# Kernel tuning notes

Hardware: AMD Instinct MI355X
Metric: run time of the kernel (lower is better)

## Reference

```python
import jax, jax.numpy as jnp
import numpy as np

B, OUT, IN = 1024, 512, 1024

def setup_inputs() -> dict:
    key = jax.random.key(0)
    k1, k2, k3, k4 = jax.random.split(key, 4)
    x = jax.random.uniform(k1, (B, IN), dtype=jnp.float32)            # inputs in [0,1]
    w = jax.random.uniform(k2, (OUT, IN), dtype=jnp.float32)          # centers in [min_input, max_input]=[0,1]
    u = jax.random.uniform(k3, (OUT, IN), dtype=jnp.float32, minval=0.2, maxval=0.7)  # slopes per init
    andor01 = jax.random.randint(k4, (1, OUT), 0, 2).astype(jnp.float32)  # frozen 0/1 mix ('*' mode)
    return {"x": x, "w": w, "u": u, "andor01": andor01}

def reference(x, w, u, andor01):
    # xuw = u * (x[b,None,i] - w[o,i]) ; z[b,o] = sum_i xuw^2 ; y = exp(-z)
    diff = u[None, :, :] * (x[:, None, :] - w[None, :, :])   # [B, OUT, IN]
    z = jnp.sum(diff * diff, axis=-1)                        # [B, OUT]
    y = jnp.exp(-z)                                          # forward of LargeAttractorExp
    # andor == '*': y + andor01 * (1 - 2y)
    return y + andor01 * (1.0 - 2.0 * y)
```

## Files before the change

kernel.cpp:

```cpp
#include <hip/hip_runtime.h>

#define B_SZ   1024
#define OUT_SZ 512
#define IN_SZ  1024
#define K2     2048
#define NKSTEP 65
#define MT     64
#define NT     32

typedef __bf16 bf16x8 __attribute__((ext_vector_type(8)));
typedef float  f32x4  __attribute__((ext_vector_type(4)));

#define A_ELEMS ((size_t)MT * NKSTEP * 64 * 8)
#define B_ELEMS ((size_t)NT * NKSTEP * 64 * 8)
#define OFF_B   (A_ELEMS * 2)
#define OFF_P   (A_ELEMS * 2 + B_ELEMS * 2)

__global__ __launch_bounds__(256) void rbf_prep_a(
    const float* __restrict__ x, __bf16* __restrict__ Ash)
{
    int t = blockIdx.x * 256 + threadIdx.x;
    int lane  = t & 63;
    int tmp   = t >> 6;
    int kStep = tmp % NKSTEP;
    int mTile = tmp / NKSTEP;
    int b     = mTile * 16 + (lane & 15);
    int quad  = lane >> 4;

    bf16x8 v;
    if (kStep < 64) {
        int kk = kStep * 32 + quad * 8;
        if (kk < IN_SZ) {
            const float4 f0 = *(const float4*)&x[(size_t)b * IN_SZ + kk];
            const float4 f1 = *(const float4*)&x[(size_t)b * IN_SZ + kk + 4];
            float f[8] = {f0.x, f0.y, f0.z, f0.w, f1.x, f1.y, f1.z, f1.w};
            #pragma unroll
            for (int j = 0; j < 8; ++j) v[j] = (__bf16)(f[j] * f[j]);
        } else {
            int i0 = kk - IN_SZ;
            const float4 f0 = *(const float4*)&x[(size_t)b * IN_SZ + i0];
            const float4 f1 = *(const float4*)&x[(size_t)b * IN_SZ + i0 + 4];
            float f[8] = {f0.x, f0.y, f0.z, f0.w, f1.x, f1.y, f1.z, f1.w};
            #pragma unroll
            for (int j = 0; j < 8; ++j) v[j] = (__bf16)f[j];
        }
    } else {
        #pragma unroll
        for (int j = 0; j < 8; ++j) v[j] = (__bf16)0.f;
        if (quad == 0) v[0] = (__bf16)1.f;
    }
    *(bf16x8*)&Ash[(size_t)t * 8] = v;
}

__global__ __launch_bounds__(256) void rbf_prep_b(
    const float* __restrict__ w, const float* __restrict__ u,
    __bf16* __restrict__ Bsh)
{
    int t = blockIdx.x * 256 + threadIdx.x;
    int lane  = t & 63;
    int tmp   = t >> 6;
    int kStep = tmp % NKSTEP;
    int nTile = tmp / NKSTEP;
    int o     = nTile * 16 + (lane & 15);
    int quad  = lane >> 4;

    bf16x8 v;
    if (kStep < 64) {
        int kk = kStep * 32 + quad * 8;
        if (kk < IN_SZ) {
            const float4 u0 = *(const float4*)&u[(size_t)o * IN_SZ + kk];
            const float4 u1 = *(const float4*)&u[(size_t)o * IN_SZ + kk + 4];
            float uf[8] = {u0.x, u0.y, u0.z, u0.w, u1.x, u1.y, u1.z, u1.w};
            #pragma unroll
            for (int j = 0; j < 8; ++j) v[j] = (__bf16)(uf[j] * uf[j]);
        } else {
            int i0 = kk - IN_SZ;
            const float4 u0 = *(const float4*)&u[(size_t)o * IN_SZ + i0];
            const float4 u1 = *(const float4*)&u[(size_t)o * IN_SZ + i0 + 4];
            const float4 w0 = *(const float4*)&w[(size_t)o * IN_SZ + i0];
            const float4 w1 = *(const float4*)&w[(size_t)o * IN_SZ + i0 + 4];
            float uf[8] = {u0.x, u0.y, u0.z, u0.w, u1.x, u1.y, u1.z, u1.w};
            float wf[8] = {w0.x, w0.y, w0.z, w0.w, w1.x, w1.y, w1.z, w1.w};
            #pragma unroll
            for (int j = 0; j < 8; ++j) v[j] = (__bf16)(-2.f * uf[j] * uf[j] * wf[j]);
        }
    } else {
        #pragma unroll
        for (int j = 0; j < 8; ++j) v[j] = (__bf16)0.f;
    }
    *(bf16x8*)&Bsh[(size_t)t * 8] = v;
}

__global__ __launch_bounds__(256) void rbf_prep_r(
    const float* __restrict__ w, const float* __restrict__ u,
    __bf16* __restrict__ Bsh)
{
    int wave = threadIdx.x >> 6;
    int lane = threadIdx.x & 63;
    int o    = blockIdx.x * 4 + wave;

    float s = 0.f;
    #pragma unroll
    for (int c = 0; c < 4; ++c) {
        int i = lane * 16 + c * 4;
        const float4 uv = *(const float4*)&u[(size_t)o * IN_SZ + i];
        const float4 wv = *(const float4*)&w[(size_t)o * IN_SZ + i];
        float t0 = uv.x * wv.x, t1 = uv.y * wv.y, t2 = uv.z * wv.z, t3 = uv.w * wv.w;
        s += t0 * t0 + t1 * t1 + t2 * t2 + t3 * t3;
    }
    #pragma unroll
    for (int d = 32; d > 0; d >>= 1) s += __shfl_down(s, d);
    if (lane == 0) {
        size_t idx = (((size_t)(o >> 4) * NKSTEP + 64) * 64 + (o & 15)) * 8;
        Bsh[idx] = (__bf16)s;
    }
}

__global__ __launch_bounds__(256) void rbf_gemm(
    const __bf16* __restrict__ Ash, const __bf16* __restrict__ Bsh,
    float* __restrict__ part)
{
    const int t    = threadIdx.x;
    const int lane = t & 63;
    const int wv   = t >> 6;
    const int mt2  = wv >> 1;
    const int nt2  = wv & 1;
    const int kz   = blockIdx.z;

    const int mTile0 = blockIdx.x * 4 + mt2 * 2;
    const int nTile0 = blockIdx.y * 4 + nt2 * 2;

    const int kLo = kz ? 33 : 0;
    const int kHi = kz ? NKSTEP : 33;

    f32x4 acc[2][2] = {};

    const __bf16* pa0 = &Ash[(((size_t)mTile0       * NKSTEP + kLo) * 64 + lane) * 8];
    const __bf16* pa1 = &Ash[(((size_t)(mTile0 + 1) * NKSTEP + kLo) * 64 + lane) * 8];
    const __bf16* pb0 = &Bsh[(((size_t)nTile0       * NKSTEP + kLo) * 64 + lane) * 8];
    const __bf16* pb1 = &Bsh[(((size_t)(nTile0 + 1) * NKSTEP + kLo) * 64 + lane) * 8];

    #pragma unroll 4
    for (int ks = kLo; ks < kHi; ++ks) {
        bf16x8 a0 = *(const bf16x8*)pa0;  pa0 += 64 * 8;
        bf16x8 a1 = *(const bf16x8*)pa1;  pa1 += 64 * 8;
        bf16x8 b0 = *(const bf16x8*)pb0;  pb0 += 64 * 8;
        bf16x8 b1 = *(const bf16x8*)pb1;  pb1 += 64 * 8;
        acc[0][0] = __builtin_amdgcn_mfma_f32_16x16x32_bf16(a0, b0, acc[0][0], 0, 0, 0);
        acc[0][1] = __builtin_amdgcn_mfma_f32_16x16x32_bf16(a0, b1, acc[0][1], 0, 0, 0);
        acc[1][0] = __builtin_amdgcn_mfma_f32_16x16x32_bf16(a1, b0, acc[1][0], 0, 0, 0);
        acc[1][1] = __builtin_amdgcn_mfma_f32_16x16x32_bf16(a1, b1, acc[1][1], 0, 0, 0);
    }

    const int quad = lane >> 4;
    #pragma unroll
    for (int mi = 0; mi < 2; ++mi) {
        int b = (mTile0 + mi) * 16 + quad * 4;
        #pragma unroll
        for (int ni = 0; ni < 2; ++ni) {
            int o = (nTile0 + ni) * 16 + (lane & 15);
            #pragma unroll
            for (int r = 0; r < 4; ++r)
                part[((size_t)kz * B_SZ + (b + r)) * OUT_SZ + o] = acc[mi][ni][r];
        }
    }
}

__global__ __launch_bounds__(256) void rbf_reduce(
    const float* __restrict__ part, const float* __restrict__ andor,
    float* __restrict__ out)
{
    int idx = blockIdx.x * 256 + threadIdx.x;
    if (idx < B_SZ * OUT_SZ) {
        float z = part[idx] + part[(size_t)B_SZ * OUT_SZ + idx];
        float a = andor[idx & (OUT_SZ - 1)];
        float y = __expf(-z);
        out[idx] = fmaf(y, 1.f - 2.f * a, a);
    }
}

extern "C" void kernel_launch(void* const* d_in, const int* in_sizes, int n_in,
                              void* d_out, int out_size, void* d_ws, size_t ws_size,
                              hipStream_t stream) {
    const float* x = (const float*)d_in[0];
    const float* w = (const float*)d_in[1];
    const float* u = (const float*)d_in[2];
    const float* a = (const float*)d_in[3];
    float* out = (float*)d_out;

    char* ws = (char*)d_ws;
    __bf16* Ash = (__bf16*)ws;
    __bf16* Bsh = (__bf16*)(ws + OFF_B);
    float*  prt = (float*)(ws + OFF_P);

    rbf_prep_a<<<dim3((MT * NKSTEP * 64) / 256), dim3(256), 0, stream>>>(x, Ash);
    rbf_prep_b<<<dim3((NT * NKSTEP * 64) / 256), dim3(256), 0, stream>>>(w, u, Bsh);
    rbf_prep_r<<<dim3(OUT_SZ / 4), dim3(256), 0, stream>>>(w, u, Bsh);

    rbf_gemm<<<dim3(B_SZ / 64, OUT_SZ / 64, 2), dim3(256), 0, stream>>>(Ash, Bsh, prt);

    rbf_reduce<<<dim3((B_SZ * OUT_SZ) / 256), dim3(256), 0, stream>>>(prt, a, out);
}
```

Before: 87.01 us.

## Merge prep kernels and fuse epilogue into GEMM, dropping split-K

Combines the three preprocessing kernels into one launch dispatched by block index. Removes the two-way split-K so each GEMM block computes the full reduction and applies exp and the andor mix directly. This eliminates the partial-sum buffer write/read and the separate reduce kernel, along with several launches. In exchange the GEMM grid halves, so fewer waves run on the device and each does twice the k-steps.

```diff
diff --git a/kernel.cpp b/kernel.cpp
--- a/kernel.cpp
+++ b/kernel.cpp
@@ -3,7 +3,6 @@
 #define B_SZ   1024
 #define OUT_SZ 512
 #define IN_SZ  1024
-#define K2     2048
 #define NKSTEP 65
 #define MT     64
 #define NT     32
@@ -14,134 +13,134 @@
 #define A_ELEMS ((size_t)MT * NKSTEP * 64 * 8)
 #define B_ELEMS ((size_t)NT * NKSTEP * 64 * 8)
 #define OFF_B   (A_ELEMS * 2)
-#define OFF_P   (A_ELEMS * 2 + B_ELEMS * 2)
 
-__global__ __launch_bounds__(256) void rbf_prep_a(
-    const float* __restrict__ x, __bf16* __restrict__ Ash)
+#define NBLK_A  (MT * NKSTEP / 4)
+#define NBLK_B  (NT * NKSTEP / 4)
+#define NBLK_R  (OUT_SZ / 4)
+
+__global__ __launch_bounds__(256) void rbf_prep(
+    const float* __restrict__ x, const float* __restrict__ w,
+    const float* __restrict__ u, __bf16* __restrict__ Ash,
+    __bf16* __restrict__ Bsh)
 {
-    int t = blockIdx.x * 256 + threadIdx.x;
-    int lane  = t & 63;
-    int tmp   = t >> 6;
-    int kStep = tmp % NKSTEP;
-    int mTile = tmp / NKSTEP;
-    int b     = mTile * 16 + (lane & 15);
-    int quad  = lane >> 4;
+    const int blk = blockIdx.x;
 
-    bf16x8 v;
-    if (kStep < 64) {
-        int kk = kStep * 32 + quad * 8;
-        if (kk < IN_SZ) {
-            const float4 f0 = *(const float4*)&x[(size_t)b * IN_SZ + kk];
-            const float4 f1 = *(const float4*)&x[(size_t)b * IN_SZ + kk + 4];
-            float f[8] = {f0.x, f0.y, f0.z, f0.w, f1.x, f1.y, f1.z, f1.w};
+    if (blk < NBLK_A) {
+        int t = blk * 256 + threadIdx.x;
+        int lane  = t & 63;
+        int tmp   = t >> 6;
+        int kStep = tmp % NKSTEP;
+        int mTile = tmp / NKSTEP;
+        int b     = mTile * 16 + (lane & 15);
+        int quad  = lane >> 4;
+
+        bf16x8 v;
+        if (kStep < 64) {
+            int kk = kStep * 32 + quad * 8;
+            if (kk < IN_SZ) {
+                const float4 f0 = *(const float4*)&x[(size_t)b * IN_SZ + kk];
+                const float4 f1 = *(const float4*)&x[(size_t)b * IN_SZ + kk + 4];
+                float f[8] = {f0.x, f0.y, f0.z, f0.w, f1.x, f1.y, f1.z, f1.w};
+                #pragma unroll
+                for (int j = 0; j < 8; ++j) v[j] = (__bf16)(f[j] * f[j]);
+            } else {
+                int i0 = kk - IN_SZ;
+                const float4 f0 = *(const float4*)&x[(size_t)b * IN_SZ + i0];
+                const float4 f1 = *(const float4*)&x[(size_t)b * IN_SZ + i0 + 4];
+                float f[8] = {f0.x, f0.y, f0.z, f0.w, f1.x, f1.y, f1.z, f1.w};
+                #pragma unroll
+                for (int j = 0; j < 8; ++j) v[j] = (__bf16)f[j];
+            }
+        } else {
             #pragma unroll
-            for (int j = 0; j < 8; ++j) v[j] = (__bf16)(f[j] * f[j]);
-        } else {
-            int i0 = kk - IN_SZ;
-            const float4 f0 = *(const float4*)&x[(size_t)b * IN_SZ + i0];
-            const float4 f1 = *(const float4*)&x[(size_t)b * IN_SZ + i0 + 4];
-            float f[8] = {f0.x, f0.y, f0.z, f0.w, f1.x, f1.y, f1.z, f1.w};
+            for (int j = 0; j < 8; ++j) v[j] = (__bf16)0.f;
+            if (quad == 0) v[0] = (__bf16)1.f;
+        }
+        *(bf16x8*)&Ash[(size_t)t * 8] = v;
+    } else if (blk < NBLK_A + NBLK_B) {
+        int t = (blk - NBLK_A) * 256 + threadIdx.x;
+        int lane  = t & 63;
+        int tmp   = t >> 6;
+        int kStep = tmp % NKSTEP;
+        int nTile = tmp / NKSTEP;
+        int o     = nTile * 16 + (lane & 15);
+        int quad  = lane >> 4;
+
+        bf16x8 v;
+        if (kStep < 64) {
+            int kk = kStep * 32 + quad * 8;
+            if (kk < IN_SZ) {
+                const float4 u0 = *(const float4*)&u[(size_t)o * IN_SZ + kk];
+                const float4 u1 = *(const float4*)&u[(size_t)o * IN_SZ + kk + 4];
+                float uf[8] = {u0.x, u0.y, u0.z, u0.w, u1.x, u1.y, u1.z, u1.w};
+                #pragma unroll
+                for (int j = 0; j < 8; ++j) v[j] = (__bf16)(uf[j] * uf[j]);
+            } else {
+                int i0 = kk - IN_SZ;
+                const float4 u0 = *(const float4*)&u[(size_t)o * IN_SZ + i0];
+                const float4 u1 = *(const float4*)&u[(size_t)o * IN_SZ + i0 + 4];
+                const float4 w0 = *(const float4*)&w[(size_t)o * IN_SZ + i0];
+                const float4 w1 = *(const float4*)&w[(size_t)o * IN_SZ + i0 + 4];
+                float uf[8] = {u0.x, u0.y, u0.z, u0.w, u1.x, u1.y, u1.z, u1.w};
+                float wf[8] = {w0.x, w0.y, w0.z, w0.w, w1.x, w1.y, w1.z, w1.w};
+                #pragma unroll
+                for (int j = 0; j < 8; ++j) v[j] = (__bf16)(-2.f * uf[j] * uf[j] * wf[j]);
+            }
+            *(bf16x8*)&Bsh[(size_t)t * 8] = v;
+        } else if (quad != 0) {
             #pragma unroll
-            for (int j = 0; j < 8; ++j) v[j] = (__bf16)f[j];
+            for (int j = 0; j < 8; ++j) v[j] = (__bf16)0.f;
+            *(bf16x8*)&Bsh[(size_t)t * 8] = v;
         }
     } else {
+        int wave = threadIdx.x >> 6;
+        int lane = threadIdx.x & 63;
+        int o    = (blk - NBLK_A - NBLK_B) * 4 + wave;
+
+        float s = 0.f;
         #pragma unroll
-        for (int j = 0; j < 8; ++j) v[j] = (__bf16)0.f;
-        if (quad == 0) v[0] = (__bf16)1.f;
-    }
-    *(bf16x8*)&Ash[(size_t)t * 8] = v;
-}
-
-__global__ __launch_bounds__(256) void rbf_prep_b(
-    const float* __restrict__ w, const float* __restrict__ u,
-    __bf16* __restrict__ Bsh)
-{
-    int t = blockIdx.x * 256 + threadIdx.x;
-    int lane  = t & 63;
-    int tmp   = t >> 6;
-    int kStep = tmp % NKSTEP;
-    int nTile = tmp / NKSTEP;
-    int o     = nTile * 16 + (lane & 15);
-    int quad  = lane >> 4;
-
-    bf16x8 v;
-    if (kStep < 64) {
-        int kk = kStep * 32 + quad * 8;
-        if (kk < IN_SZ) {
-            const float4 u0 = *(const float4*)&u[(size_t)o * IN_SZ + kk];
-            const float4 u1 = *(const float4*)&u[(size_t)o * IN_SZ + kk + 4];
-            float uf[8] = {u0.x, u0.y, u0.z, u0.w, u1.x, u1.y, u1.z, u1.w};
+        for (int c = 0; c < 4; ++c) {
+            int i = lane * 16 + c * 4;
+            const float4 uv = *(const float4*)&u[(size_t)o * IN_SZ + i];
+            const float4 wv = *(const float4*)&w[(size_t)o * IN_SZ + i];
+            float t0 = uv.x * wv.x, t1 = uv.y * wv.y, t2 = uv.z * wv.z, t3 = uv.w * wv.w;
+            s += t0 * t0 + t1 * t1 + t2 * t2 + t3 * t3;
+        }
+        #pragma unroll
+        for (int d = 32; d > 0; d >>= 1) s += __shfl_down(s, d);
+        if (lane == 0) {
+            bf16x8 vr;
             #pragma unroll
-            for (int j = 0; j < 8; ++j) v[j] = (__bf16)(uf[j] * uf[j]);
-        } else {
-            int i0 = kk - IN_SZ;
-            const float4 u0 = *(const float4*)&u[(size_t)o * IN_SZ + i0];
-            const float4 u1 = *(const float4*)&u[(size_t)o * IN_SZ + i0 + 4];
-            const float4 w0 = *(const float4*)&w[(size_t)o * IN_SZ + i0];
-            const float4 w1 = *(const float4*)&w[(size_t)o * IN_SZ + i0 + 4];
-            float uf[8] = {u0.x, u0.y, u0.z, u0.w, u1.x, u1.y, u1.z, u1.w};
-            float wf[8] = {w0.x, w0.y, w0.z, w0.w, w1.x, w1.y, w1.z, w1.w};
-            #pragma unroll
-            for (int j = 0; j < 8; ++j) v[j] = (__bf16)(-2.f * uf[j] * uf[j] * wf[j]);
+            for (int j = 0; j < 8; ++j) vr[j] = (__bf16)0.f;
+            vr[0] = (__bf16)s;
+            size_t idx = ((size_t)(o >> 4) * NKSTEP + 64) * 64 + (o & 15);
+            *(bf16x8*)&Bsh[idx * 8] = vr;
         }
-    } else {
-        #pragma unroll
-        for (int j = 0; j < 8; ++j) v[j] = (__bf16)0.f;
-    }
-    *(bf16x8*)&Bsh[(size_t)t * 8] = v;
-}
-
-__global__ __launch_bounds__(256) void rbf_prep_r(
-    const float* __restrict__ w, const float* __restrict__ u,
-    __bf16* __restrict__ Bsh)
-{
-    int wave = threadIdx.x >> 6;
-    int lane = threadIdx.x & 63;
-    int o    = blockIdx.x * 4 + wave;
-
-    float s = 0.f;
-    #pragma unroll
-    for (int c = 0; c < 4; ++c) {
-        int i = lane * 16 + c * 4;
-        const float4 uv = *(const float4*)&u[(size_t)o * IN_SZ + i];
-        const float4 wv = *(const float4*)&w[(size_t)o * IN_SZ + i];
-        float t0 = uv.x * wv.x, t1 = uv.y * wv.y, t2 = uv.z * wv.z, t3 = uv.w * wv.w;
-        s += t0 * t0 + t1 * t1 + t2 * t2 + t3 * t3;
-    }
-    #pragma unroll
-    for (int d = 32; d > 0; d >>= 1) s += __shfl_down(s, d);
-    if (lane == 0) {
-        size_t idx = (((size_t)(o >> 4) * NKSTEP + 64) * 64 + (o & 15)) * 8;
-        Bsh[idx] = (__bf16)s;
     }
 }
 
 __global__ __launch_bounds__(256) void rbf_gemm(
     const __bf16* __restrict__ Ash, const __bf16* __restrict__ Bsh,
-    float* __restrict__ part)
+    const float* __restrict__ andor, float* __restrict__ out)
 {
     const int t    = threadIdx.x;
     const int lane = t & 63;
     const int wv   = t >> 6;
     const int mt2  = wv >> 1;
     const int nt2  = wv & 1;
-    const int kz   = blockIdx.z;
 
     const int mTile0 = blockIdx.x * 4 + mt2 * 2;
     const int nTile0 = blockIdx.y * 4 + nt2 * 2;
 
-    const int kLo = kz ? 33 : 0;
-    const int kHi = kz ? NKSTEP : 33;
-
     f32x4 acc[2][2] = {};
 
-    const __bf16* pa0 = &Ash[(((size_t)mTile0       * NKSTEP + kLo) * 64 + lane) * 8];
-    const __bf16* pa1 = &Ash[(((size_t)(mTile0 + 1) * NKSTEP + kLo) * 64 + lane) * 8];
-    const __bf16* pb0 = &Bsh[(((size_t)nTile0       * NKSTEP + kLo) * 64 + lane) * 8];
-    const __bf16* pb1 = &Bsh[(((size_t)(nTile0 + 1) * NKSTEP + kLo) * 64 + lane) * 8];
+    const __bf16* pa0 = &Ash[(((size_t)mTile0       * NKSTEP) * 64 + lane) * 8];
+    const __bf16* pa1 = &Ash[(((size_t)(mTile0 + 1) * NKSTEP) * 64 + lane) * 8];
+    const __bf16* pb0 = &Bsh[(((size_t)nTile0       * NKSTEP) * 64 + lane) * 8];
+    const __bf16* pb1 = &Bsh[(((size_t)(nTile0 + 1) * NKSTEP) * 64 + lane) * 8];
 
-    #pragma unroll 4
-    for (int ks = kLo; ks < kHi; ++ks) {
+    #pragma unroll 5
+    for (int ks = 0; ks < NKSTEP; ++ks) {
         bf16x8 a0 = *(const bf16x8*)pa0;  pa0 += 64 * 8;
         bf16x8 a1 = *(const bf16x8*)pa1;  pa1 += 64 * 8;
         bf16x8 b0 = *(const bf16x8*)pb0;  pb0 += 64 * 8;
@@ -154,28 +153,19 @@
 
     const int quad = lane >> 4;
     #pragma unroll
-    for (int mi = 0; mi < 2; ++mi) {
-        int b = (mTile0 + mi) * 16 + quad * 4;
+    for (int ni = 0; ni < 2; ++ni) {
+        int o = (nTile0 + ni) * 16 + (lane & 15);
+        float a  = andor[o];
+        float s1 = 1.f - 2.f * a;
         #pragma unroll
-        for (int ni = 0; ni < 2; ++ni) {
-            int o = (nTile0 + ni) * 16 + (lane & 15);
+        for (int mi = 0; mi < 2; ++mi) {
+            int b = (mTile0 + mi) * 16 + quad * 4;
             #pragma unroll
-            for (int r = 0; r < 4; ++r)
-                part[((size_t)kz * B_SZ + (b + r)) * OUT_SZ + o] = acc[mi][ni][r];
+            for (int r = 0; r < 4; ++r) {
+                float y = __expf(-acc[mi][ni][r]);
+                out[(size_t)(b + r) * OUT_SZ + o] = fmaf(y, s1, a);
+            }
         }
-    }
-}
-
-__global__ __launch_bounds__(256) void rbf_reduce(
-    const float* __restrict__ part, const float* __restrict__ andor,
-    float* __restrict__ out)
-{
-    int idx = blockIdx.x * 256 + threadIdx.x;
-    if (idx < B_SZ * OUT_SZ) {
-        float z = part[idx] + part[(size_t)B_SZ * OUT_SZ + idx];
-        float a = andor[idx & (OUT_SZ - 1)];
-        float y = __expf(-z);
-        out[idx] = fmaf(y, 1.f - 2.f * a, a);
     }
 }
 
@@ -191,13 +181,7 @@
     char* ws = (char*)d_ws;
     __bf16* Ash = (__bf16*)ws;
     __bf16* Bsh = (__bf16*)(ws + OFF_B);
-    float*  prt = (float*)(ws + OFF_P);
 
-    rbf_prep_a<<<dim3((MT * NKSTEP * 64) / 256), dim3(256), 0, stream>>>(x, Ash);
-    rbf_prep_b<<<dim3((NT * NKSTEP * 64) / 256), dim3(256), 0, stream>>>(w, u, Bsh);
-    rbf_prep_r<<<dim3(OUT_SZ / 4), dim3(256), 0, stream>>>(w, u, Bsh);
-
-    rbf_gemm<<<dim3(B_SZ / 64, OUT_SZ / 64, 2), dim3(256), 0, stream>>>(Ash, Bsh, prt);
-
-    rbf_reduce<<<dim3((B_SZ * OUT_SZ) / 256), dim3(256), 0, stream>>>(prt, a, out);
+    rbf_prep<<<dim3(NBLK_A + NBLK_B + NBLK_R), dim3(256), 0, stream>>>(x, w, u, Ash, Bsh);
+    rbf_gemm<<<dim3(B_SZ / 64, OUT_SZ / 64), dim3(256), 0, stream>>>(Ash, Bsh, a, out);
 }
```

Result: no change. 86.57 us (-0.5%).
